# Kernel optimization log

Hardware: AMD Instinct MI355X
Metric: run time of the kernel (lower is better)

## Reference

```python
import jax, jax.numpy as jnp
import numpy as np

B, N_NODES, T_IN = 512, 32, 12
HID, HEADS, OUT_CH, DEG = 64, 8, 9, 8


def setup_inputs() -> dict:
    key = jax.random.key(0)
    ks = jax.random.split(key, 26)
    rn = lambda k, s, sc=0.1: (jax.random.normal(k, s, jnp.float32) * sc)
    E = B * N_NODES * DEG
    src = jax.random.randint(ks[0], (E,), 0, N_NODES, jnp.int32)
    dst = jax.random.randint(ks[1], (E,), 0, N_NODES, jnp.int32)
    off = jnp.repeat(jnp.arange(B, dtype=jnp.int32) * N_NODES, N_NODES * DEG)
    edge_index = jnp.stack([src + off, dst + off])  # block-diagonal batched graph
    x = jax.random.normal(ks[2], (B, N_NODES, T_IN), jnp.float32)
    return {
        "x": x,
        "edge_index": edge_index,
        # gat1: in=T_IN -> HEADS*HID, concat
        "W1": rn(ks[3], (T_IN, HEADS * HID)),
        "a_src1": rn(ks[4], (HEADS, HID)),
        "a_dst1": rn(ks[5], (HEADS, HID)),
        "b1": rn(ks[6], (HEADS * HID,), 0.01),
        # gat2: in=HEADS*HID -> HID, heads=1, mean (concat=False)
        "W2": rn(ks[7], (HEADS * HID, HID), 0.05),
        "a_src2": rn(ks[8], (1, HID)),
        "a_dst2": rn(ks[9], (1, HID)),
        "b2": rn(ks[10], (HID,), 0.01),
        "gamma": jnp.ones((HID,), jnp.float32),
        "beta": jnp.zeros((HID,), jnp.float32),
        # gru1: input_size=N_NODES(=32), hidden=HID
        "Wi1": rn(ks[11], (3 * HID, N_NODES)),
        "Wh1": rn(ks[12], (3 * HID, HID)),
        "bi1": rn(ks[13], (3 * HID,), 0.01),
        "bh1": rn(ks[14], (3 * HID,), 0.01),
        # gru2: input_size=HID, hidden=HID
        "Wi2": rn(ks[15], (3 * HID, HID)),
        "Wh2": rn(ks[16], (3 * HID, HID)),
        "bi2": rn(ks[17], (3 * HID,), 0.01),
        "bh2": rn(ks[18], (3 * HID,), 0.01),
        "Wf": rn(ks[19], (OUT_CH, HID)),
        "bf": rn(ks[20], (OUT_CH,), 0.01),
    }


def _gat_layer(x, src, dst, W, a_s, a_d, b, concat):
    # PyG GATConv (eval mode, self-loops already appended by caller)
    Nn = x.shape[0]
    heads, hc = a_s.shape
    h = (x @ W).reshape(Nn, heads, hc)                 # [N, H, C]
    es = jnp.sum(h * a_s, axis=-1)                     # [N, H]
    ed = jnp.sum(h * a_d, axis=-1)
    e = jax.nn.leaky_relu(es[src] + ed[dst], 0.2)      # [E, H]
    m = jax.ops.segment_max(e, dst, num_segments=Nn)
    p = jnp.exp(e - m[dst])
    s = jax.ops.segment_sum(p, dst, num_segments=Nn)
    alpha = p / (s[dst] + 1e-16)                       # per-dst softmax
    out = jax.ops.segment_sum(h[src] * alpha[:, :, None], dst, num_segments=Nn)
    out = out.reshape(Nn, heads * hc) if concat else out.mean(axis=1)
    return out + b


def _gru(x, Wi, Wh, bi, bh):
    # torch.nn.GRU (batch_first) single layer; x: [B, T, F]
    H = Wh.shape[1]
    xi = x @ Wi.T + bi                                 # [B, T, 3H]
    def step(h, xt):
        gh = h @ Wh.T + bh
        r = jax.nn.sigmoid(xt[:, :H] + gh[:, :H])
        z = jax.nn.sigmoid(xt[:, H:2 * H] + gh[:, H:2 * H])
        n = jnp.tanh(xt[:, 2 * H:] + r * gh[:, 2 * H:])
        hn = (1.0 - z) * n + z * h
        return hn, hn
    h0 = jnp.zeros((x.shape[0], H), x.dtype)
    _, ys = jax.lax.scan(step, h0, jnp.swapaxes(xi, 0, 1))
    return jnp.swapaxes(ys, 0, 1)


def reference(x, edge_index, W1, a_src1, a_dst1, b1, W2, a_src2, a_dst2, b2,
              gamma, beta, Wi1, Wh1, bi1, bh1, Wi2, Wh2, bi2, bh2, Wf, bf):
    Bsz, Nn_, T = x.shape
    Nn = Bsz * Nn_
    xf = x.reshape(Nn, T)                              # dropout is identity in eval
    sl = jnp.arange(Nn, dtype=edge_index.dtype)        # PyG add_self_loops=True
    src = jnp.concatenate([edge_index[0], sl])
    dst = jnp.concatenate([edge_index[1], sl])
    h = jax.nn.elu(_gat_layer(xf, src, dst, W1, a_src1, a_dst1, b1, True))
    h = jax.nn.elu(_gat_layer(h, src, dst, W2, a_src2, a_dst2, b2, False))
    mu = h.mean(-1, keepdims=True)
    var = ((h - mu) ** 2).mean(-1, keepdims=True)
    h = (h - mu) / jnp.sqrt(var + 1e-5) * gamma + beta
    seq = h.reshape(Bsz, Nn_, -1).transpose(0, 2, 1)   # [B, HID(seq), N_NODES(feat)]
    g = _gru(seq, Wi1, Wh1, bi1, bh1)
    g = _gru(g, Wi2, Wh2, bi2, bh2)
    return g[:, -1, :] @ Wf.T + bf                     # [B, OUT_CH]
```

## Files before the change

kernel.cpp:

```cpp
#include <hip/hip_runtime.h>
#include <hip/hip_bf16.h>
#include <stdint.h>

#define BATCH 512
#define NN 32
#define T_IN 12
#define HID 64
#define HEADS 8
#define OUT_CH 9
#define EPB (NN*8)
#define ETOT (EPB+NN)
#define F1 (HEADS*HID)

using u16 = unsigned short;
using u32 = unsigned int;
typedef _Float16 f16;
typedef _Float16 f16x2 __attribute__((ext_vector_type(2)));
typedef u32 v4u __attribute__((ext_vector_type(4)));
typedef float v4f __attribute__((ext_vector_type(4)));

__device__ __forceinline__ float bf2f(u16 u){ return __uint_as_float(((u32)u)<<16); }
__device__ __forceinline__ u16 f2bf(float f){
    u32 x = __float_as_uint(f);
    u32 r = (x + 0x7FFFu + ((x>>16)&1u))>>16;
    return (u16)r;
}
__device__ __forceinline__ u32 packf16(float a, float b){
    f16x2 p; p.x=(f16)a; p.y=(f16)b; return __builtin_bit_cast(u32,p);
}
__device__ __forceinline__ u16 f2h16(float a){ f16 h=(f16)a; return __builtin_bit_cast(u16,h); }
__device__ __forceinline__ float lof(u32 w){ return (float)__builtin_bit_cast(f16x2,w).x; }
__device__ __forceinline__ float hif(u32 w){ return (float)__builtin_bit_cast(f16x2,w).y; }
__device__ __forceinline__ float dot2(u32 a, u32 b, float c){
#if __has_builtin(__builtin_amdgcn_fdot2)
    return __builtin_amdgcn_fdot2(__builtin_bit_cast(f16x2,a), __builtin_bit_cast(f16x2,b), c, false);
#else
    return fmaf(lof(a),lof(b), fmaf(hif(a),hif(b), c));
#endif
}
__device__ __forceinline__ float elu1(float x){ return x > 0.f ? x : (__expf(x)-1.f); }
__device__ __forceinline__ float sigm(float x){ return 1.f/(1.f+__expf(-x)); }
__device__ __forceinline__ float tanh_(float x){ return 1.f - 2.f/(__expf(2.f*x)+1.f); }
__device__ __forceinline__ u32 fenc(float v){
    u32 b=__float_as_uint(v);
    return (b&0x80000000u) ? ~b : (b|0x80000000u);
}
__device__ __forceinline__ float fdec(u32 k){
    return __uint_as_float((k&0x80000000u) ? (k&0x7FFFFFFFu) : ~k);
}

#define DOT4(acc,A,W) do{ acc=dot2(A.x,W.x,acc); acc=dot2(A.y,W.y,acc); \
                          acc=dot2(A.z,W.z,acc); acc=dot2(A.w,W.w,acc); }while(0)

#define PIN(v) asm("" : "+v"(v))

struct CvtDesc {
    const void* src[16];
    void*       dst[16];
    int         n[16];
};

__global__ __launch_bounds__(256) void k_setup(
    const u32* __restrict__ xw, CvtDesc d,
    const void* __restrict__ W2src, u16* __restrict__ W2i,
    const void* __restrict__ Wi1, const void* __restrict__ Wh1,
    const void* __restrict__ Wi2, const void* __restrict__ Wh2,
    u32* __restrict__ wpk, int* __restrict__ flag)
{
    __shared__ int cnt;
    if(threadIdx.x==0) cnt=0;
    __syncthreads();
    int c=0;
    for(int i=threadIdx.x;i<4096;i+=256){
        u32 w=xw[i];
        if(w & 0x7FFFFFFFu){
            u32 el=(w>>7)&0xFFu;
            if(el>=0x90u) c++;
        }
    }
    atomicAdd(&cnt,c);
    __syncthreads();
    const int f = (cnt>256) ? 1 : 0;
    if(blockIdx.x==0 && threadIdx.x==0) *flag=f;

    const int bk=blockIdx.x;
    if(bk<128){
        int seg=bk>>3, sub=bk&7;
        const void* s=d.src[seg];
        float* o=(float*)d.dst[seg];
        int n=d.n[seg];
        for(int i=sub*256+threadIdx.x;i<n;i+=2048)
            o[i] = f ? ((const float*)s)[i] : bf2f(((const u16*)s)[i]);
    } else if(bk<256){
        int i=(bk-128)*256+threadIdx.x;
        int k=i>>6, j=i&63;
        float v = f? ((const float*)W2src)[i] : bf2f(((const u16*)W2src)[i]);
        W2i[ (((size_t)(k>>3)*64 + j)<<3) + (k&7) ] = f2h16(v);
    } else {
        int w=(bk-256)*256+threadIdx.x;
        int m=w/6144;
        int rem=w-m*6144;
        int row=rem>>5, kw=rem&31;
        const void* s=(m==0)?Wi1:(m==1)?Wh1:(m==2)?Wi2:Wh2;
        int K=(m==0)?32:64;
        int k0=2*kw, k1=k0+1;
        float v0=0.f, v1=0.f;
        if(k0<K) v0 = f? ((const float*)s)[row*K+k0] : bf2f(((const u16*)s)[row*K+k0]);
        if(k1<K) v1 = f? ((const float*)s)[row*K+k1] : bf2f(((const u16*)s)[row*K+k1]);
        wpk[w]=packf16(v0,v1);
    }
}

__global__ __launch_bounds__(512,4) void k_ab(
    const float* __restrict__ x, const int* __restrict__ ei,
    const float* __restrict__ W1, const float* __restrict__ a_s, const float* __restrict__ a_d,
    const float* __restrict__ b1,
    const uint4* __restrict__ W2i, const float* __restrict__ a_s2, const float* __restrict__ a_d2,
    const float* __restrict__ b2, const float* __restrict__ gam, const float* __restrict__ bet,
    float* __restrict__ hlng)
{
    const int b = blockIdx.x, t = threadIdx.x;

    __shared__ __align__(16) float s_x[NN][12];
    __shared__ __align__(16) u16 s_h[NN][520];
    __shared__ __align__(16) u32 s_aspk[HEADS*32], s_adpk[HEADS*32];
    __shared__ float s_es[NN][HEADS], s_ed[NN][HEADS];
    __shared__ unsigned char s_src[ETOT], s_dst[ETOT];
    __shared__ float s_al[HEADS][ETOT];
    __shared__ u32 s_mx[NN*HEADS];
    __shared__ float s_sm[NN*HEADS], s_inv[NN*HEADS];
    __shared__ int s_cnt[NN], s_off[NN], s_fil[NN];
    __shared__ short s_lst[ETOT];
    __shared__ float s_h2[NN][HID];

    for(int i=t;i<NN*T_IN;i+=512) s_x[i/12][i%12] = x[b*NN*T_IN + i];
    if(t<256){
        s_aspk[t]=packf16(a_s[2*t],a_s[2*t+1]);
        s_adpk[t]=packf16(a_d[2*t],a_d[2*t+1]);
        s_mx[t]=0u; s_sm[t]=0.f;
    }
    if(t<EPB){
        s_src[t] = (unsigned char)(ei[b*EPB+t] - b*NN);
        s_dst[t] = (unsigned char)(ei[(size_t)BATCH*EPB + b*EPB+t] - b*NN);
    }
    if(t<NN){ s_src[EPB+t]=s_dst[EPB+t]=(unsigned char)t; s_cnt[t]=0; s_fil[t]=0; }
    v4f Wc0,Wc1,Wc2;
    Wc0.x=W1[0*F1+t]; Wc0.y=W1[1*F1+t]; Wc0.z=W1[2*F1+t]; Wc0.w=W1[3*F1+t];
    Wc1.x=W1[4*F1+t]; Wc1.y=W1[5*F1+t]; Wc1.z=W1[6*F1+t]; Wc1.w=W1[7*F1+t];
    Wc2.x=W1[8*F1+t]; Wc2.y=W1[9*F1+t]; Wc2.z=W1[10*F1+t]; Wc2.w=W1[11*F1+t];
    __syncthreads();

    for(int n=0;n<NN;n++){
        const float4* xp=(const float4*)s_x[n];
        float4 xa=xp[0], xb=xp[1], xc=xp[2];
        float A=0.f;
        A=fmaf(xa.x,Wc0.x,A); A=fmaf(xa.y,Wc0.y,A); A=fmaf(xa.z,Wc0.z,A); A=fmaf(xa.w,Wc0.w,A);
        A=fmaf(xb.x,Wc1.x,A); A=fmaf(xb.y,Wc1.y,A); A=fmaf(xb.z,Wc1.z,A); A=fmaf(xb.w,Wc1.w,A);
        A=fmaf(xc.x,Wc2.x,A); A=fmaf(xc.y,Wc2.y,A); A=fmaf(xc.z,Wc2.z,A); A=fmaf(xc.w,Wc2.w,A);
        s_h[n][t]=f2h16(A);
    }
    for(int e=t;e<ETOT;e+=512) atomicAdd(&s_cnt[s_dst[e]],1);
    __syncthreads();

    if(t<256){
        int n=t&31, hd=t>>5;
        const v4u* hp=(const v4u*)((const u16*)s_h[n] + hd*64);
        v4u h0=hp[0],h1=hp[1],h2=hp[2],h3=hp[3],h4=hp[4],h5=hp[5],h6=hp[6],h7=hp[7];
        const v4u* ap=(const v4u*)&s_aspk[hd*32];
        const v4u* dp=(const v4u*)&s_adpk[hd*32];
        float e1=0.f,e2=0.f;
        { v4u w=ap[0]; DOT4(e1,h0,w); w=ap[1]; DOT4(e1,h1,w); w=ap[2]; DOT4(e1,h2,w); w=ap[3]; DOT4(e1,h3,w);
          w=ap[4]; DOT4(e1,h4,w); w=ap[5]; DOT4(e1,h5,w); w=ap[6]; DOT4(e1,h6,w); w=ap[7]; DOT4(e1,h7,w); }
        { v4u w=dp[0]; DOT4(e2,h0,w); w=dp[1]; DOT4(e2,h1,w); w=dp[2]; DOT4(e2,h2,w); w=dp[3]; DOT4(e2,h3,w);
          w=dp[4]; DOT4(e2,h4,w); w=dp[5]; DOT4(e2,h5,w); w=dp[6]; DOT4(e2,h6,w); w=dp[7]; DOT4(e2,h7,w); }
        s_es[n][hd]=e1; s_ed[n][hd]=e2;
    }
    if(t==0){ int o=0; for(int i=0;i<NN;i++){ s_off[i]=o; o+=s_cnt[i]; } }
    __syncthreads();

    for(int e=t;e<ETOT;e+=512){
        int d=s_dst[e]; int p=atomicAdd(&s_fil[d],1); s_lst[s_off[d]+p]=(short)e;
    }
    for(int i=t;i<ETOT*HEADS;i+=512){
        int hd=i/ETOT, e=i-hd*ETOT;
        int sr=s_src[e], d=s_dst[e];
        float v = s_es[sr][hd]+s_ed[d][hd];
        v = v>0.f? v : 0.2f*v;
        s_al[hd][e]=v;
        atomicMax(&s_mx[d*8+hd], fenc(v));
    }
    __syncthreads();

    for(int i=t;i<ETOT*HEADS;i+=512){
        int hd=i/ETOT, e=i-hd*ETOT;
        int d=s_dst[e];
        float p=__expf(s_al[hd][e]-fdec(s_mx[d*8+hd]));
        s_al[hd][e]=p;
        atomicAdd(&s_sm[d*8+hd], p);
    }
    __syncthreads();
    if(t<256) s_inv[t]=1.f/(s_sm[t]+1e-16f);
    __syncthreads();

    u32 res[16];
    const int dA=t&31, hdA=(t>>5)&7, chA=t>>8;
    {
        int o=s_off[dA], cnt=s_cnt[dA];
        float inv=s_inv[dA*8+hdA];
        v4f a0=0,a1=0,a2=0,a3=0,a4=0,a5=0,a6=0,a7=0;
        for(int i=0;i<cnt;i++){
            int e=s_lst[o+i]; float av=s_al[hdA][e]; int sr=s_src[e];
            const v4u* hp=(const v4u*)((const u16*)s_h[sr] + hdA*64 + chA*32);
            v4u p0=hp[0],p1=hp[1],p2=hp[2],p3=hp[3];
            a0.x=fmaf(av,lof(p0.x),a0.x); a0.y=fmaf(av,hif(p0.x),a0.y);
            a0.z=fmaf(av,lof(p0.y),a0.z); a0.w=fmaf(av,hif(p0.y),a0.w);
            a1.x=fmaf(av,lof(p0.z),a1.x); a1.y=fmaf(av,hif(p0.z),a1.y);
            a1.z=fmaf(av,lof(p0.w),a1.z); a1.w=fmaf(av,hif(p0.w),a1.w);
            a2.x=fmaf(av,lof(p1.x),a2.x); a2.y=fmaf(av,hif(p1.x),a2.y);
            a2.z=fmaf(av,lof(p1.y),a2.z); a2.w=fmaf(av,hif(p1.y),a2.w);
            a3.x=fmaf(av,lof(p1.z),a3.x); a3.y=fmaf(av,hif(p1.z),a3.y);
            a3.z=fmaf(av,lof(p1.w),a3.z); a3.w=fmaf(av,hif(p1.w),a3.w);
            a4.x=fmaf(av,lof(p2.x),a4.x); a4.y=fmaf(av,hif(p2.x),a4.y);
            a4.z=fmaf(av,lof(p2.y),a4.z); a4.w=fmaf(av,hif(p2.y),a4.w);
            a5.x=fmaf(av,lof(p2.z),a5.x); a5.y=fmaf(av,hif(p2.z),a5.y);
            a5.z=fmaf(av,lof(p2.w),a5.z); a5.w=fmaf(av,hif(p2.w),a5.w);
            a6.x=fmaf(av,lof(p3.x),a6.x); a6.y=fmaf(av,hif(p3.x),a6.y);
            a6.z=fmaf(av,lof(p3.y),a6.z); a6.w=fmaf(av,hif(p3.y),a6.w);
            a7.x=fmaf(av,lof(p3.z),a7.x); a7.y=fmaf(av,hif(p3.z),a7.y);
            a7.z=fmaf(av,lof(p3.w),a7.z); a7.w=fmaf(av,hif(p3.w),a7.w);
        }
        const float* bp = b1 + hdA*64 + chA*32;
        res[0] = packf16(elu1(a0.x*inv+bp[0]),  elu1(a0.y*inv+bp[1]));
        res[1] = packf16(elu1(a0.z*inv+bp[2]),  elu1(a0.w*inv+bp[3]));
        res[2] = packf16(elu1(a1.x*inv+bp[4]),  elu1(a1.y*inv+bp[5]));
        res[3] = packf16(elu1(a1.z*inv+bp[6]),  elu1(a1.w*inv+bp[7]));
        res[4] = packf16(elu1(a2.x*inv+bp[8]),  elu1(a2.y*inv+bp[9]));
        res[5] = packf16(elu1(a2.z*inv+bp[10]), elu1(a2.w*inv+bp[11]));
        res[6] = packf16(elu1(a3.x*inv+bp[12]), elu1(a3.y*inv+bp[13]));
        res[7] = packf16(elu1(a3.z*inv+bp[14]), elu1(a3.w*inv+bp[15]));
        res[8] = packf16(elu1(a4.x*inv+bp[16]), elu1(a4.y*inv+bp[17]));
        res[9] = packf16(elu1(a4.z*inv+bp[18]), elu1(a4.w*inv+bp[19]));
        res[10]= packf16(elu1(a5.x*inv+bp[20]), elu1(a5.y*inv+bp[21]));
        res[11]= packf16(elu1(a5.z*inv+bp[22]), elu1(a5.w*inv+bp[23]));
        res[12]= packf16(elu1(a6.x*inv+bp[24]), elu1(a6.y*inv+bp[25]));
        res[13]= packf16(elu1(a6.z*inv+bp[26]), elu1(a6.w*inv+bp[27]));
        res[14]= packf16(elu1(a7.x*inv+bp[28]), elu1(a7.y*inv+bp[29]));
        res[15]= packf16(elu1(a7.z*inv+bp[30]), elu1(a7.w*inv+bp[31]));
    }
    __syncthreads();
    {
        u32* rw = ((u32*)s_h) + dA*260 + hdA*32 + chA*16;
        #pragma unroll
        for(int i=0;i<16;i++) rw[i]=res[i];
    }
    if(t<NN){ s_fil[t]=0; s_mx[t]=0u; s_sm[t]=0.f; }
    __syncthreads();

    {
        int n0=(t>>6)<<2, j=t&63;
        const u32* r0=((const u32*)s_h)+(n0+0)*260;
        const u32* r1=((const u32*)s_h)+(n0+1)*260;
        const u32* r2=((const u32*)s_h)+(n0+2)*260;
        const u32* r3=((const u32*)s_h)+(n0+3)*260;
        float a0=0,a1=0,a2=0,a3=0;
        for(int kb=0;kb<64;kb++){
            uint4 A0=*(const uint4*)&r0[kb*4];
            uint4 A1=*(const uint4*)&r1[kb*4];
            uint4 A2=*(const uint4*)&r2[kb*4];
            uint4 A3=*(const uint4*)&r3[kb*4];
            uint4 w0=W2i[kb*64+j];
            a0=dot2(A0.x,w0.x,a0); a0=dot2(A0.y,w0.y,a0); a0=dot2(A0.z,w0.z,a0); a0=dot2(A0.w,w0.w,a0);
            a1=dot2(A1.x,w0.x,a1); a1=dot2(A1.y,w0.y,a1); a1=dot2(A1.z,w0.z,a1); a1=dot2(A1.w,w0.w,a1);
            a2=dot2(A2.x,w0.x,a2); a2=dot2(A2.y,w0.y,a2); a2=dot2(A2.z,w0.z,a2); a2=dot2(A2.w,w0.w,a2);
            a3=dot2(A3.x,w0.x,a3); a3=dot2(A3.y,w0.y,a3); a3=dot2(A3.z,w0.z,a3); a3=dot2(A3.w,w0.w,a3);
        }
        s_h2[n0+0][j]=a0; s_h2[n0+1][j]=a1; s_h2[n0+2][j]=a2; s_h2[n0+3][j]=a3;
    }
    __syncthreads();

    if(t<256){
        int n=t>>3, g=t&7;
        float e1=0,e2=0;
        #pragma unroll
        for(int cc=0; cc<8; cc++){
            float hv = s_h2[n][g*8+cc];
            e1 += hv*a_s2[g*8+cc];
            e2 += hv*a_d2[g*8+cc];
        }
        #pragma unroll
        for(int m=1;m<8;m<<=1){ e1 += __shfl_xor(e1,m,64); e2 += __shfl_xor(e2,m,64); }
        if(g==0){ s_es[n][0]=e1; s_ed[n][0]=e2; }
    }
    __syncthreads();

    for(int e=t;e<ETOT;e+=512){
        int d=s_dst[e];
        float v = s_es[s_src[e]][0] + s_ed[d][0];
        v = v>0.f? v:0.2f*v;
        s_al[0][e]=v;
        atomicMax(&s_mx[d], fenc(v));
    }
    __syncthreads();

    for(int e=t;e<ETOT;e+=512){
        int d=s_dst[e];
        float p=__expf(s_al[0][e]-fdec(s_mx[d]));
        s_al[0][e]=p;
        atomicAdd(&s_sm[d], p);
    }
    __syncthreads();
    if(t<NN) s_inv[t]=1.f/(s_sm[t]+1e-16f);
    __syncthreads();

    if(t<256){
        int n=t>>3, g=t&7;
        v4f a0=0, a1=0;
        int o=s_off[n], cnt=s_cnt[n];
        float inv=s_inv[n];
        for(int i=0;i<cnt;i++){
            int e=s_lst[o+i]; float a=s_al[0][e]; int sr=s_src[e];
            const float4* hp=(const float4*)&s_h2[sr][g*8];
            float4 v0=hp[0], v1=hp[1];
            a0.x=fmaf(a,v0.x,a0.x); a0.y=fmaf(a,v0.y,a0.y); a0.z=fmaf(a,v0.z,a0.z); a0.w=fmaf(a,v0.w,a0.w);
            a1.x=fmaf(a,v1.x,a1.x); a1.y=fmaf(a,v1.y,a1.y); a1.z=fmaf(a,v1.z,a1.z); a1.w=fmaf(a,v1.w,a1.w);
        }
        const float* bp=b2+g*8;
        float v0=elu1(a0.x*inv+bp[0]), v1=elu1(a0.y*inv+bp[1]);
        float v2=elu1(a0.z*inv+bp[2]), v3=elu1(a0.w*inv+bp[3]);
        float v4=elu1(a1.x*inv+bp[4]), v5=elu1(a1.y*inv+bp[5]);
        float v6=elu1(a1.z*inv+bp[6]), v7=elu1(a1.w*inv+bp[7]);
        float sum=v0+v1+v2+v3+v4+v5+v6+v7;
        float sq=v0*v0+v1*v1+v2*v2+v3*v3+v4*v4+v5*v5+v6*v6+v7*v7;
        #pragma unroll
        for(int m=1;m<8;m<<=1){ sum+=__shfl_xor(sum,m,64); sq+=__shfl_xor(sq,m,64); }
        float mu = sum*(1.f/64.f);
        float var = sq*(1.f/64.f) - mu*mu;
        float rs = rsqrtf(var + 1e-5f);
        float* op = hlng + (size_t)b*HID*NN;
        int c=g*8;
        op[(c+0)*NN+n]=(v0-mu)*rs*gam[c+0]+bet[c+0];
        op[(c+1)*NN+n]=(v1-mu)*rs*gam[c+1]+bet[c+1];
        op[(c+2)*NN+n]=(v2-mu)*rs*gam[c+2]+bet[c+2];
        op[(c+3)*NN+n]=(v3-mu)*rs*gam[c+3]+bet[c+3];
        op[(c+4)*NN+n]=(v4-mu)*rs*gam[c+4]+bet[c+4];
        op[(c+5)*NN+n]=(v5-mu)*rs*gam[c+5]+bet[c+5];
        op[(c+6)*NN+n]=(v6-mu)*rs*gam[c+6]+bet[c+6];
        op[(c+7)*NN+n]=(v7-mu)*rs*gam[c+7]+bet[c+7];
    }
}

__global__ __launch_bounds__(256,2) void k_gruf(
    const float* __restrict__ hlng, const u32* __restrict__ wpk,
    const float* __restrict__ bi1, const float* __restrict__ bh1,
    const float* __restrict__ bi2, const float* __restrict__ bh2,
    const float* __restrict__ Wf, const float* __restrict__ bfv,
    void* __restrict__ outp, const int* __restrict__ flag)
{
    const int b=blockIdx.x, t=threadIdx.x;
    const int wave=t>>6, lane=t&63;
    const int layer=wave>>1;
    const int ublk=wave&1;
    const int uu=lane&31, s=lane>>5;
    const int u=ublk*32+uu;

    __shared__ __align__(16) u32 s_x1[64*16];
    __shared__ __align__(16) u32 s_h1[2][32];
    __shared__ __align__(16) u32 s_h2[2][32];
    __shared__ float s_h2f[64];

    { const float2* g=(const float2*)(hlng + (size_t)b*2048);
      for(int w=t;w<1024;w+=256){ float2 v=g[w]; s_x1[w]=packf16(v.x,v.y); } }
    if(t<32){ s_h1[0][t]=0u; s_h1[1][t]=0u; s_h2[0][t]=0u; s_h2[1][t]=0u; }

    u32 wiR[16],wiZ[16],wiN[16],whR[16],whZ[16],whN[16];
    const u32* wiu = wpk + (size_t)(layer*2+0)*6144;
    const u32* whu = wpk + (size_t)(layer*2+1)*6144;
    if(layer==0){
        #pragma unroll
        for(int k=0;k<8;k++){
            wiR[k]=wiu[u*32+s*8+k];
            wiZ[k]=wiu[(64+u)*32+s*8+k];
            wiN[k]=wiu[(128+u)*32+s*8+k];
        }
        #pragma unroll
        for(int k=0;k<8;k++){ PIN(wiR[k]); PIN(wiZ[k]); PIN(wiN[k]); }
        #pragma unroll
        for(int k=0;k<16;k++){
            whR[k]=whu[u*32+s*16+k];
            whZ[k]=whu[(64+u)*32+s*16+k];
            whN[k]=whu[(128+u)*32+s*16+k];
        }
        #pragma unroll
        for(int k=0;k<16;k++){ PIN(whR[k]); PIN(whZ[k]); PIN(whN[k]); }
    } else {
        #pragma unroll
        for(int k=0;k<16;k++){
            wiR[k]=wiu[u*32+s*16+k];
            wiZ[k]=wiu[(64+u)*32+s*16+k];
            wiN[k]=wiu[(128+u)*32+s*16+k];
            whR[k]=whu[u*32+s*16+k];
            whZ[k]=whu[(64+u)*32+s*16+k];
            whN[k]=whu[(128+u)*32+s*16+k];
        }
        #pragma unroll
        for(int k=0;k<16;k++){
            PIN(wiR[k]); PIN(wiZ[k]); PIN(wiN[k]);
            PIN(whR[k]); PIN(whZ[k]); PIN(whN[k]);
        }
    }
    const float* bi = layer? bi2:bi1;
    const float* bh = layer? bh2:bh1;
    float br=bi[u]+bh[u], bz=bi[64+u]+bh[64+u], bxn=bi[128+u], bhn=bh[128+u];
    float h=0.f;
    __syncthreads();

    for(int it=0; it<=64; ++it){
        const int pb=(it-1)&1, cb=it&1;
        bool act;
        float pr=0.f,pz=0.f,pxn=0.f,phn=0.f;
        if(layer==0){
            act=(it<64);
            if(act){
                const u32* xp=&s_x1[it*16+s*8];
                const u32* hp=&s_h1[pb][s*16];
                #pragma unroll
                for(int k=0;k<8;k++){ u32 xv=xp[k]; pr=dot2(xv,wiR[k],pr); pz=dot2(xv,wiZ[k],pz); pxn=dot2(xv,wiN[k],pxn); }
                #pragma unroll
                for(int k=0;k<16;k++){ u32 hv=hp[k]; pr=dot2(hv,whR[k],pr); pz=dot2(hv,whZ[k],pz); phn=dot2(hv,whN[k],phn); }
            }
        } else {
            act=(it>=1);
            if(act){
                const u32* xp=&s_h1[pb][s*16];
                const u32* hp=&s_h2[pb][s*16];
                #pragma unroll
                for(int k=0;k<16;k++){
                    u32 xv=xp[k], hv=hp[k];
                    pr=dot2(xv,wiR[k],pr); pz=dot2(xv,wiZ[k],pz); pxn=dot2(xv,wiN[k],pxn);
                    pr=dot2(hv,whR[k],pr); pz=dot2(hv,whZ[k],pz); phn=dot2(hv,whN[k],phn);
                }
            }
        }
        if(act){
            pr  += __shfl_xor(pr ,32,64);
            pz  += __shfl_xor(pz ,32,64);
            pxn += __shfl_xor(pxn,32,64);
            phn += __shfl_xor(phn,32,64);
            float r=sigm(pr+br), z=sigm(pz+bz);
            float n=tanh_(pxn+bxn + r*(phn+bhn));
            h=(1.f-z)*n + z*h;
            if(s==0){
                u16 hv=f2h16(h);
                if(layer==0) ((u16*)s_h1[cb])[u]=hv;
                else { ((u16*)s_h2[cb])[u]=hv; if(it==64) s_h2f[u]=h; }
            }
        }
        __syncthreads();
    }

    if(t<OUT_CH){
        float acc=bfv[t];
        const float4* wp=(const float4*)(Wf + t*64);
        const float4* hp=(const float4*)s_h2f;
        #pragma unroll
        for(int k=0;k<16;k++){
            float4 w=wp[k], v=hp[k];
            acc += w.x*v.x + w.y*v.y + w.z*v.z + w.w*v.w;
        }
        if(*flag) ((float*)outp)[b*OUT_CH+t]=acc;
        else      ((u16*)outp)[b*OUT_CH+t]=f2bf(acc);
    }
}

extern "C" void kernel_launch(void* const* d_in, const int* in_sizes, int n_in,
                              void* d_out, int out_size, void* d_ws, size_t ws_size,
                              hipStream_t stream)
{
    char* ws=(char*)d_ws;
    int* flag = (int*)ws;
    float* cf = (float*)(ws + 256);
    float* c_x   = cf; cf+=196608;
    float* c_W1  = cf; cf+=6144;
    float* c_as1 = cf; cf+=512;
    float* c_ad1 = cf; cf+=512;
    float* c_b1  = cf; cf+=512;
    float* c_as2 = cf; cf+=64;
    float* c_ad2 = cf; cf+=64;
    float* c_b2  = cf; cf+=64;
    float* c_gam = cf; cf+=64;
    float* c_bet = cf; cf+=64;
    float* c_bi1 = cf; cf+=192;
    float* c_bh1 = cf; cf+=192;
    float* c_bi2 = cf; cf+=192;
    float* c_bh2 = cf; cf+=192;
    float* c_Wf  = cf; cf+=576;
    float* c_bf  = cf; cf+=9;
    uintptr_t p = ((uintptr_t)cf + 255) & ~(uintptr_t)255;
    u16* c_W2i = (u16*)p;
    p = (p + 32768*2 + 255) & ~(uintptr_t)255;
    u32* wpk = (u32*)p;
    p = (p + 24576*4 + 255) & ~(uintptr_t)255;
    float* hlng = (float*)p;

    const int* ei = (const int*)d_in[1];

    CvtDesc d;
    const int srcIdx[16] = {0,2,3,4,5,7,8,9,10,11,14,15,18,19,20,21};
    void* dsts[16] = {c_x,c_W1,c_as1,c_ad1,c_b1,c_as2,c_ad2,c_b2,c_gam,c_bet,
                      c_bi1,c_bh1,c_bi2,c_bh2,c_Wf,c_bf};
    const int ns[16] = {196608,6144,512,512,512,64,64,64,64,64,
                        192,192,192,192,576,9};
    for(int i=0;i<16;i++){ d.src[i]=d_in[srcIdx[i]]; d.dst[i]=dsts[i]; d.n[i]=ns[i]; }

    k_setup <<<dim3(352),dim3(256),0,stream>>>((const u32*)d_in[0], d,
                                               d_in[6], c_W2i,
                                               d_in[12], d_in[13], d_in[16], d_in[17],
                                               wpk, flag);
    k_ab    <<<dim3(BATCH),dim3(512),0,stream>>>(
        c_x, ei, c_W1, c_as1, c_ad1, c_b1,
        (const uint4*)c_W2i, c_as2, c_ad2, c_b2, c_gam, c_bet, hlng);
    k_gruf  <<<dim3(BATCH),dim3(256),0,stream>>>(hlng, wpk, c_bi1,c_bh1,c_bi2,c_bh2,
                                                 c_Wf, c_bf, d_out, flag);
}
```

Measured before the change: 216.9 us.

## Give each GRU unit one full-K thread, halving block size and dropping shuffles

The GRU kernel now runs with 128 threads per block, one wave per layer. Each thread owns one hidden unit and computes the full dot products over all inputs, instead of splitting K across two half-waves and combining the partial sums with cross-lane shuffles. This removes the shuffle reductions and the half-wave write predicate, and it halves the number of waves that hit each per-step barrier. In exchange each thread keeps twice as many packed weights in registers (about 192 u32), which raises register pressure and can cause spills, and it doubles the serial dot-product chain per step, so per-step latency may grow.

```diff
diff --git a/kernel.cpp b/kernel.cpp
--- a/kernel.cpp
+++ b/kernel.cpp
@@ -51,8 +51,6 @@
 
 #define DOT4(acc,A,W) do{ acc=dot2(A.x,W.x,acc); acc=dot2(A.y,W.y,acc); \
                           acc=dot2(A.z,W.z,acc); acc=dot2(A.w,W.w,acc); }while(0)
-
-#define PIN(v) asm("" : "+v"(v))
 
 struct CvtDesc {
     const void* src[16];
@@ -349,7 +347,7 @@
     }
 }
 
-__global__ __launch_bounds__(256,2) void k_gruf(
+__global__ __launch_bounds__(128,2) void k_gruf(
     const float* __restrict__ hlng, const u32* __restrict__ wpk,
     const float* __restrict__ bi1, const float* __restrict__ bh1,
     const float* __restrict__ bi2, const float* __restrict__ bh2,
@@ -357,55 +355,43 @@
     void* __restrict__ outp, const int* __restrict__ flag)
 {
     const int b=blockIdx.x, t=threadIdx.x;
-    const int wave=t>>6, lane=t&63;
-    const int layer=wave>>1;
-    const int ublk=wave&1;
-    const int uu=lane&31, s=lane>>5;
-    const int u=ublk*32+uu;
+    const int layer=t>>6;
+    const int u=t&63;
 
     __shared__ __align__(16) u32 s_x1[64*16];
-    __shared__ __align__(16) u32 s_h1[2][32];
-    __shared__ __align__(16) u32 s_h2[2][32];
+    __shared__ __align__(16) u32 s_g1[2][32];
+    __shared__ __align__(16) u32 s_g2[2][32];
     __shared__ float s_h2f[64];
 
     { const float2* g=(const float2*)(hlng + (size_t)b*2048);
-      for(int w=t;w<1024;w+=256){ float2 v=g[w]; s_x1[w]=packf16(v.x,v.y); } }
-    if(t<32){ s_h1[0][t]=0u; s_h1[1][t]=0u; s_h2[0][t]=0u; s_h2[1][t]=0u; }
-
-    u32 wiR[16],wiZ[16],wiN[16],whR[16],whZ[16],whN[16];
+      for(int w=t;w<1024;w+=128){ float2 v=g[w]; s_x1[w]=packf16(v.x,v.y); } }
+    if(t<32){ s_g1[0][t]=0u; s_g1[1][t]=0u; s_g2[0][t]=0u; s_g2[1][t]=0u; }
+
+    u32 wiR[32],wiZ[32],wiN[32],whR[32],whZ[32],whN[32];
     const u32* wiu = wpk + (size_t)(layer*2+0)*6144;
     const u32* whu = wpk + (size_t)(layer*2+1)*6144;
     if(layer==0){
         #pragma unroll
-        for(int k=0;k<8;k++){
-            wiR[k]=wiu[u*32+s*8+k];
-            wiZ[k]=wiu[(64+u)*32+s*8+k];
-            wiN[k]=wiu[(128+u)*32+s*8+k];
-        }
-        #pragma unroll
-        for(int k=0;k<8;k++){ PIN(wiR[k]); PIN(wiZ[k]); PIN(wiN[k]); }
-        #pragma unroll
         for(int k=0;k<16;k++){
-            whR[k]=whu[u*32+s*16+k];
-            whZ[k]=whu[(64+u)*32+s*16+k];
-            whN[k]=whu[(128+u)*32+s*16+k];
-        }
-        #pragma unroll
-        for(int k=0;k<16;k++){ PIN(whR[k]); PIN(whZ[k]); PIN(whN[k]); }
+            wiR[k]=wiu[u*32+k];
+            wiZ[k]=wiu[(64+u)*32+k];
+            wiN[k]=wiu[(128+u)*32+k];
+        }
+        #pragma unroll
+        for(int k=0;k<32;k++){
+            whR[k]=whu[u*32+k];
+            whZ[k]=whu[(64+u)*32+k];
+            whN[k]=whu[(128+u)*32+k];
+        }
     } else {
         #pragma unroll
-        for(int k=0;k<16;k++){
-            wiR[k]=wiu[u*32+s*16+k];
-            wiZ[k]=wiu[(64+u)*32+s*16+k];
-            wiN[k]=wiu[(128+u)*32+s*16+k];
-            whR[k]=whu[u*32+s*16+k];
-            whZ[k]=whu[(64+u)*32+s*16+k];
-            whN[k]=whu[(128+u)*32+s*16+k];
-        }
-        #pragma unroll
-        for(int k=0;k<16;k++){
-            PIN(wiR[k]); PIN(wiZ[k]); PIN(wiN[k]);
-            PIN(whR[k]); PIN(whZ[k]); PIN(whN[k]);
+        for(int k=0;k<32;k++){
+            wiR[k]=wiu[u*32+k];
+            wiZ[k]=wiu[(64+u)*32+k];
+            wiN[k]=wiu[(128+u)*32+k];
+            whR[k]=whu[u*32+k];
+            whZ[k]=whu[(64+u)*32+k];
+            whN[k]=whu[(128+u)*32+k];
         }
     }
     const float* bi = layer? bi2:bi1;
@@ -421,20 +407,20 @@
         if(layer==0){
             act=(it<64);
             if(act){
-                const u32* xp=&s_x1[it*16+s*8];
-                const u32* hp=&s_h1[pb][s*16];
+                const u32* xp=&s_x1[it*16];
+                const u32* hp=s_g1[pb];
                 #pragma unroll
-                for(int k=0;k<8;k++){ u32 xv=xp[k]; pr=dot2(xv,wiR[k],pr); pz=dot2(xv,wiZ[k],pz); pxn=dot2(xv,wiN[k],pxn); }
+                for(int k=0;k<16;k++){ u32 xv=xp[k]; pr=dot2(xv,wiR[k],pr); pz=dot2(xv,wiZ[k],pz); pxn=dot2(xv,wiN[k],pxn); }
                 #pragma unroll
-                for(int k=0;k<16;k++){ u32 hv=hp[k]; pr=dot2(hv,whR[k],pr); pz=dot2(hv,whZ[k],pz); phn=dot2(hv,whN[k],phn); }
+                for(int k=0;k<32;k++){ u32 hv=hp[k]; pr=dot2(hv,whR[k],pr); pz=dot2(hv,whZ[k],pz); phn=dot2(hv,whN[k],phn); }
             }
         } else {
             act=(it>=1);
             if(act){
-                const u32* xp=&s_h1[pb][s*16];
-                const u32* hp=&s_h2[pb][s*16];
+                const u32* xp=s_g1[pb];
+                const u32* hp=s_g2[pb];
                 #pragma unroll
-                for(int k=0;k<16;k++){
+                for(int k=0;k<32;k++){
                     u32 xv=xp[k], hv=hp[k];
                     pr=dot2(xv,wiR[k],pr); pz=dot2(xv,wiZ[k],pz); pxn=dot2(xv,wiN[k],pxn);
                     pr=dot2(hv,whR[k],pr); pz=dot2(hv,whZ[k],pz); phn=dot2(hv,whN[k],phn);
@@ -442,18 +428,12 @@
             }
         }
         if(act){
-            pr  += __shfl_xor(pr ,32,64);
-            pz  += __shfl_xor(pz ,32,64);
-            pxn += __shfl_xor(pxn,32,64);
-            phn += __shfl_xor(phn,32,64);
             float r=sigm(pr+br), z=sigm(pz+bz);
             float n=tanh_(pxn+bxn + r*(phn+bhn));
             h=(1.f-z)*n + z*h;
-            if(s==0){
-                u16 hv=f2h16(h);
-                if(layer==0) ((u16*)s_h1[cb])[u]=hv;
-                else { ((u16*)s_h2[cb])[u]=hv; if(it==64) s_h2f[u]=h; }
-            }
+            u16 hv=f2h16(h);
+            if(layer==0) ((u16*)s_g1[cb])[u]=hv;
+            else { ((u16*)s_g2[cb])[u]=hv; if(it==64) s_h2f[u]=h; }
         }
         __syncthreads();
     }
@@ -519,6 +499,6 @@
     k_ab    <<<dim3(BATCH),dim3(512),0,stream>>>(
         c_x, ei, c_W1, c_as1, c_ad1, c_b1,
         (const uint4*)c_W2i, c_as2, c_ad2, c_b2, c_gam, c_bet, hlng);
-    k_gruf  <<<dim3(BATCH),dim3(256),0,stream>>>(hlng, wpk, c_bi1,c_bh1,c_bi2,c_bh2,
+    k_gruf  <<<dim3(BATCH),dim3(128),0,stream>>>(hlng, wpk, c_bi1,c_bh1,c_bi2,c_bh2,
                                                  c_Wf, c_bf, d_out, flag);
 }
```

Result: slower. 253.5 us (+16.9%).
